# Optimization experiments

Hardware: AMD Instinct MI355X
Metric: run time of the kernel (lower is better)

The kernel has to match this reference:

```python
import jax, jax.numpy as jnp
import numpy as np

B, D, N = 1024, 512, 256
INIT_RANGE = 0.5

def setup_inputs() -> dict:
    key = jax.random.key(0)
    kx, kc, kd = jax.random.split(key, 3)
    x = jax.random.uniform(kx, (B, D), dtype=jnp.float32)
    W_con = INIT_RANGE * jax.random.uniform(kc, (N, D), dtype=jnp.float32)
    W_dis = INIT_RANGE * jax.random.uniform(kd, (N, D), dtype=jnp.float32)
    return {"x": x, "W_con": W_con, "W_dis": W_dis}

def _log_prod(X):
    # Product.forward: y = -1 / (-1 + sum(log(X), dim=1)); X: (B, D, N) -> (B, N)
    return -1.0 / (-1.0 + jnp.sum(jnp.log(X), axis=1))

def reference(x, W_con, W_dis):
    # Conjunction: prod-like over 1 - (1-x) * w  (broadcast to (B, D, N))
    con = _log_prod(1.0 - (1.0 - x)[:, :, None] * W_con.T)
    # Disjunction: 1 - prod-like over 1 - x * w
    dis = 1.0 - _log_prod(1.0 - x[:, :, None] * W_dis.T)
    return jnp.concatenate([con, dis], axis=1)  # (B, 2N)
```

## Files before the change

kernel.cpp:

```cpp
#include <hip/hip_runtime.h>


#define DDIM 512
#define NTOT 512
#define NHALF 256
#define BM 64
#define BN 32
#define BK 32
#define BKP 36

__global__ __launch_bounds__(256) void union_kernel(
    const float* __restrict__ x,
    const float* __restrict__ Wc,
    const float* __restrict__ Wd,
    float* __restrict__ out)
{
    __shared__ float xs[BM * BKP];
    __shared__ float ws[BN * BKP];

    const int tid   = threadIdx.x;
    const int ntile = blockIdx.x;
    const int btile = blockIdx.y;
    const int n0    = ntile * BN;
    const int b0    = btile * BM;
    const bool isCon = (n0 < NHALF);

    const float csel = isCon ? -1.0f : 1.0f;
    const float coff = isCon ?  1.0f : 0.0f;
    const float* Wbase = isCon ? (Wc + n0 * DDIM) : (Wd + (n0 - NHALF) * DDIM);

    const int srow = tid >> 3;
    const int sc4  = (tid & 7) * 4;

    const int tb = tid >> 4;
    const int tn = tid & 15;

    float4 xr0, xr1, wr0;
    auto load_tile = [&](int d0) {
        xr0 = *reinterpret_cast<const float4*>(&x[(b0 + srow) * DDIM + d0 + sc4]);
        xr1 = *reinterpret_cast<const float4*>(&x[(b0 + srow + 32) * DDIM + d0 + sc4]);
        wr0 = *reinterpret_cast<const float4*>(&Wbase[srow * DDIM + d0 + sc4]);
    };

    float prod[4][2], acc[4][2];
#pragma unroll
    for (int i = 0; i < 4; ++i)
#pragma unroll
        for (int j = 0; j < 2; ++j) { prod[i][j] = 1.0f; acc[i][j] = 0.0f; }

    load_tile(0);

    constexpr int NT = DDIM / BK;
#pragma unroll 1
    for (int t = 0; t < NT; ++t) {
        float4 u0, u1;
        u0.x = fmaf(csel, xr0.x, coff); u0.y = fmaf(csel, xr0.y, coff);
        u0.z = fmaf(csel, xr0.z, coff); u0.w = fmaf(csel, xr0.w, coff);
        u1.x = fmaf(csel, xr1.x, coff); u1.y = fmaf(csel, xr1.y, coff);
        u1.z = fmaf(csel, xr1.z, coff); u1.w = fmaf(csel, xr1.w, coff);
        *reinterpret_cast<float4*>(&xs[srow * BKP + sc4])        = u0;
        *reinterpret_cast<float4*>(&xs[(srow + 32) * BKP + sc4]) = u1;
        *reinterpret_cast<float4*>(&ws[srow * BKP + sc4])        = wr0;
        __syncthreads();

        if (t + 1 < NT) load_tile((t + 1) * BK);

#pragma unroll
        for (int k4 = 0; k4 < BK; k4 += 4) {
            float4 uu[4], wv[2];
#pragma unroll
            for (int i = 0; i < 4; ++i)
                uu[i] = *reinterpret_cast<const float4*>(&xs[(tb * 4 + i) * BKP + k4]);
#pragma unroll
            for (int j = 0; j < 2; ++j)
                wv[j] = *reinterpret_cast<const float4*>(&ws[(tn * 2 + j) * BKP + k4]);
#pragma unroll
            for (int i = 0; i < 4; ++i)
#pragma unroll
                for (int j = 0; j < 2; ++j) {
                    prod[i][j] *= fmaf(-uu[i].x, wv[j].x, 1.0f);
                    prod[i][j] *= fmaf(-uu[i].y, wv[j].y, 1.0f);
                    prod[i][j] *= fmaf(-uu[i].z, wv[j].z, 1.0f);
                    prod[i][j] *= fmaf(-uu[i].w, wv[j].w, 1.0f);
                }
        }

#pragma unroll
        for (int i = 0; i < 4; ++i)
#pragma unroll
            for (int j = 0; j < 2; ++j) {
                acc[i][j] += __log2f(prod[i][j]);
                prod[i][j] = 1.0f;
            }
        __syncthreads();
    }

    constexpr float LN2 = 0.69314718055994530942f;
#pragma unroll
    for (int i = 0; i < 4; ++i) {
        const int b = b0 + tb * 4 + i;
        float2 v;
        {
            const float S0 = acc[i][0] * LN2;
            const float r0 = 1.0f / (1.0f - S0);
            v.x = isCon ? r0 : 1.0f - r0;
        }
        {
            const float S1 = acc[i][1] * LN2;
            const float r1 = 1.0f / (1.0f - S1);
            v.y = isCon ? r1 : 1.0f - r1;
        }
        *reinterpret_cast<float2*>(&out[b * NTOT + n0 + tn * 2]) = v;
    }
}

extern "C" void kernel_launch(void* const* d_in, const int* in_sizes, int n_in,
                              void* d_out, int out_size, void* d_ws, size_t ws_size,
                              hipStream_t stream) {
    const float* x  = (const float*)d_in[0];
    const float* Wc = (const float*)d_in[1];
    const float* Wd = (const float*)d_in[2];
    float* out = (float*)d_out;
    dim3 grid(NTOT / BN, 1024 / BM);
    union_kernel<<<grid, 256, 0, stream>>>(x, Wc, Wd, out);
}
```

Measured before the change: 81.58 us.

## Split reduction dimension across blocks with workspace partials and a second reduce pass

Replaces the single kernel that looped over all of D with a split-K scheme. Eight blocks along z each handle a 64-wide D slice and write log2 partial sums to a workspace. A second kernel sums the partials and applies the final reciprocal transform. Tiles grow to 64x64 with a 4x4 per-thread micro-tile, which raises the grid from 256 to 1024 blocks for better CU occupancy. The cost is 16 MB of workspace traffic, an extra launch, and uncoalesced scalar stores in pass 1.

```diff
diff --git a/kernel.cpp b/kernel.cpp
--- a/kernel.cpp
+++ b/kernel.cpp
@@ -5,113 +5,108 @@
 #define NTOT 512
 #define NHALF 256
 #define BM 64
-#define BN 32
-#define BK 32
-#define BKP 36
+#define BN 64
+#define BK 64
+#define KS 8
+#define P  68
+#define SLICE (1024 * 512)
 
-__global__ __launch_bounds__(256) void union_kernel(
+__global__ __launch_bounds__(256) void union_pass1(
     const float* __restrict__ x,
     const float* __restrict__ Wc,
     const float* __restrict__ Wd,
-    float* __restrict__ out)
+    float* __restrict__ ws)
 {
-    __shared__ float xs[BM * BKP];
-    __shared__ float ws[BN * BKP];
+    __shared__ float xs[BM * P];
+    __shared__ float wsh[BN * P];
 
-    const int tid   = threadIdx.x;
-    const int ntile = blockIdx.x;
-    const int btile = blockIdx.y;
-    const int n0    = ntile * BN;
-    const int b0    = btile * BM;
+    const int tid = threadIdx.x;
+    const int n0  = blockIdx.x * BN;
+    const int b0  = blockIdx.y * BM;
+    const int d0  = blockIdx.z * BK;
     const bool isCon = (n0 < NHALF);
-
     const float csel = isCon ? -1.0f : 1.0f;
     const float coff = isCon ?  1.0f : 0.0f;
-    const float* Wbase = isCon ? (Wc + n0 * DDIM) : (Wd + (n0 - NHALF) * DDIM);
+    const float* Wb = isCon ? (Wc + n0 * DDIM) : (Wd + (n0 - NHALF) * DDIM);
 
-    const int srow = tid >> 3;
-    const int sc4  = (tid & 7) * 4;
+#pragma unroll
+    for (int i = 0; i < 4; ++i) {
+        const int f   = i * 256 + tid;
+        const int row = f >> 4;
+        const int c4  = (f & 15) * 4;
+        float4 xv = *reinterpret_cast<const float4*>(&x[(b0 + row) * DDIM + d0 + c4]);
+        float4 u;
+        u.x = fmaf(csel, xv.x, coff);
+        u.y = fmaf(csel, xv.y, coff);
+        u.z = fmaf(csel, xv.z, coff);
+        u.w = fmaf(csel, xv.w, coff);
+        *reinterpret_cast<float4*>(&xs[row * P + c4]) = u;
+        float4 wv = *reinterpret_cast<const float4*>(&Wb[row * DDIM + d0 + c4]);
+        *reinterpret_cast<float4*>(&wsh[row * P + c4]) = wv;
+    }
+    __syncthreads();
 
     const int tb = tid >> 4;
     const int tn = tid & 15;
 
-    float4 xr0, xr1, wr0;
-    auto load_tile = [&](int d0) {
-        xr0 = *reinterpret_cast<const float4*>(&x[(b0 + srow) * DDIM + d0 + sc4]);
-        xr1 = *reinterpret_cast<const float4*>(&x[(b0 + srow + 32) * DDIM + d0 + sc4]);
-        wr0 = *reinterpret_cast<const float4*>(&Wbase[srow * DDIM + d0 + sc4]);
-    };
-
-    float prod[4][2], acc[4][2];
+    float prod[4][4];
 #pragma unroll
     for (int i = 0; i < 4; ++i)
 #pragma unroll
-        for (int j = 0; j < 2; ++j) { prod[i][j] = 1.0f; acc[i][j] = 0.0f; }
+        for (int j = 0; j < 4; ++j) prod[i][j] = 1.0f;
 
-    load_tile(0);
-
-    constexpr int NT = DDIM / BK;
-#pragma unroll 1
-    for (int t = 0; t < NT; ++t) {
-        float4 u0, u1;
-        u0.x = fmaf(csel, xr0.x, coff); u0.y = fmaf(csel, xr0.y, coff);
-        u0.z = fmaf(csel, xr0.z, coff); u0.w = fmaf(csel, xr0.w, coff);
-        u1.x = fmaf(csel, xr1.x, coff); u1.y = fmaf(csel, xr1.y, coff);
-        u1.z = fmaf(csel, xr1.z, coff); u1.w = fmaf(csel, xr1.w, coff);
-        *reinterpret_cast<float4*>(&xs[srow * BKP + sc4])        = u0;
-        *reinterpret_cast<float4*>(&xs[(srow + 32) * BKP + sc4]) = u1;
-        *reinterpret_cast<float4*>(&ws[srow * BKP + sc4])        = wr0;
-        __syncthreads();
-
-        if (t + 1 < NT) load_tile((t + 1) * BK);
-
+#pragma unroll 4
+    for (int k4 = 0; k4 < 16; ++k4) {
+        const int kk = k4 * 4;
+        float4 uu[4], wv[4];
 #pragma unroll
-        for (int k4 = 0; k4 < BK; k4 += 4) {
-            float4 uu[4], wv[2];
+        for (int i = 0; i < 4; ++i)
+            uu[i] = *reinterpret_cast<const float4*>(&xs[(tb + 16 * i) * P + kk]);
 #pragma unroll
-            for (int i = 0; i < 4; ++i)
-                uu[i] = *reinterpret_cast<const float4*>(&xs[(tb * 4 + i) * BKP + k4]);
-#pragma unroll
-            for (int j = 0; j < 2; ++j)
-                wv[j] = *reinterpret_cast<const float4*>(&ws[(tn * 2 + j) * BKP + k4]);
-#pragma unroll
-            for (int i = 0; i < 4; ++i)
-#pragma unroll
-                for (int j = 0; j < 2; ++j) {
-                    prod[i][j] *= fmaf(-uu[i].x, wv[j].x, 1.0f);
-                    prod[i][j] *= fmaf(-uu[i].y, wv[j].y, 1.0f);
-                    prod[i][j] *= fmaf(-uu[i].z, wv[j].z, 1.0f);
-                    prod[i][j] *= fmaf(-uu[i].w, wv[j].w, 1.0f);
-                }
-        }
-
+        for (int j = 0; j < 4; ++j)
+            wv[j] = *reinterpret_cast<const float4*>(&wsh[(tn + 16 * j) * P + kk]);
 #pragma unroll
         for (int i = 0; i < 4; ++i)
 #pragma unroll
-            for (int j = 0; j < 2; ++j) {
-                acc[i][j] += __log2f(prod[i][j]);
-                prod[i][j] = 1.0f;
+            for (int j = 0; j < 4; ++j) {
+                prod[i][j] *= fmaf(-uu[i].x, wv[j].x, 1.0f);
+                prod[i][j] *= fmaf(-uu[i].y, wv[j].y, 1.0f);
+                prod[i][j] *= fmaf(-uu[i].z, wv[j].z, 1.0f);
+                prod[i][j] *= fmaf(-uu[i].w, wv[j].w, 1.0f);
             }
-        __syncthreads();
     }
 
+    float* dst = ws + (size_t)blockIdx.z * SLICE;
+#pragma unroll
+    for (int i = 0; i < 4; ++i)
+#pragma unroll
+        for (int j = 0; j < 4; ++j)
+            dst[(b0 + tb + 16 * i) * NTOT + (n0 + tn + 16 * j)] = __log2f(prod[i][j]);
+}
+
+__global__ __launch_bounds__(256) void union_pass2(
+    const float* __restrict__ ws, float* __restrict__ out)
+{
+    const int i = blockIdx.x * 256 + threadIdx.x;
+    const float4* w4 = reinterpret_cast<const float4*>(ws);
+    float4 s = w4[i];
+#pragma unroll
+    for (int k = 1; k < KS; ++k) {
+        const float4 t = w4[(size_t)k * (SLICE / 4) + i];
+        s.x += t.x; s.y += t.y; s.z += t.z; s.w += t.w;
+    }
     constexpr float LN2 = 0.69314718055994530942f;
-#pragma unroll
-    for (int i = 0; i < 4; ++i) {
-        const int b = b0 + tb * 4 + i;
-        float2 v;
-        {
-            const float S0 = acc[i][0] * LN2;
-            const float r0 = 1.0f / (1.0f - S0);
-            v.x = isCon ? r0 : 1.0f - r0;
-        }
-        {
-            const float S1 = acc[i][1] * LN2;
-            const float r1 = 1.0f / (1.0f - S1);
-            v.y = isCon ? r1 : 1.0f - r1;
-        }
-        *reinterpret_cast<float2*>(&out[b * NTOT + n0 + tn * 2]) = v;
+    const int col = (i * 4) & (NTOT - 1);
+    const bool con = col < NHALF;
+    float4 o;
+    o.x = 1.0f / (1.0f - s.x * LN2);
+    o.y = 1.0f / (1.0f - s.y * LN2);
+    o.z = 1.0f / (1.0f - s.z * LN2);
+    o.w = 1.0f / (1.0f - s.w * LN2);
+    if (!con) {
+        o.x = 1.0f - o.x; o.y = 1.0f - o.y; o.z = 1.0f - o.z; o.w = 1.0f - o.w;
     }
+    reinterpret_cast<float4*>(out)[i] = o;
 }
 
 extern "C" void kernel_launch(void* const* d_in, const int* in_sizes, int n_in,
@@ -121,6 +116,9 @@
     const float* Wc = (const float*)d_in[1];
     const float* Wd = (const float*)d_in[2];
     float* out = (float*)d_out;
-    dim3 grid(NTOT / BN, 1024 / BM);
-    union_kernel<<<grid, 256, 0, stream>>>(x, Wc, Wd, out);
+    float* ws  = (float*)d_ws;
+
+    dim3 g1(NTOT / BN, 1024 / BM, KS);
+    union_pass1<<<g1, 256, 0, stream>>>(x, Wc, Wd, ws);
+    union_pass2<<<(SLICE / 4) / 256, 256, 0, stream>>>(ws, out);
 }
```

New measurement: 81.74 us. About the same (+0.2%).
